# Kernel optimization log

Measured on AMD Instinct MI355X. Metric: run time of the kernel, lower is better.

Reference implementation:

```python
import jax, jax.numpy as jnp
import numpy as np

B, T, C, H, HS = 4, 2048, 384, 6, 64
EPS = 1e-5


def setup_inputs() -> dict:
    key = jax.random.key(0)
    ks = jax.random.split(key, 8)
    s = lambda fan_in: 1.0 / np.sqrt(fan_in)
    return {
        "x": jax.random.normal(ks[0], (B, T, C), jnp.float32),
        "wq": jax.random.normal(ks[1], (H, C, HS), jnp.float32) * s(C),
        "wk": jax.random.normal(ks[2], (H, C, HS), jnp.float32) * s(C),
        "wv": jax.random.normal(ks[3], (H, C, HS), jnp.float32) * s(C),
        "w_proj": jax.random.normal(ks[4], (C, C), jnp.float32) * s(C),
        "b_proj": jnp.zeros((C,), jnp.float32),
        "w1": jax.random.normal(ks[5], (C, 4 * C), jnp.float32) * s(C),
        "b1": jnp.zeros((4 * C,), jnp.float32),
        "w2": jax.random.normal(ks[6], (4 * C, C), jnp.float32) * s(4 * C),
        "b2": jnp.zeros((C,), jnp.float32),
        "g1": jnp.ones((C,), jnp.float32),
        "be1": jnp.zeros((C,), jnp.float32),
        "g2": jnp.ones((C,), jnp.float32),
        "be2": jnp.zeros((C,), jnp.float32),
    }


def _layernorm(z, g, b):
    m = jnp.mean(z, axis=-1, keepdims=True)
    v = jnp.mean((z - m) ** 2, axis=-1, keepdims=True)
    return (z - m) * jax.lax.rsqrt(v + EPS) * g + b


def reference(x, wq, wk, wv, w_proj, b_proj, w1, b1, w2, b2, g1, be1, g2, be2):
    Bx, Tx, Cx = x.shape
    h = _layernorm(x, g1, be1)
    # per-head projections, no bias
    q = jnp.einsum('btc,hcd->bhtd', h, wq)
    k = jnp.einsum('btc,hcd->bhtd', h, wk)
    v = jnp.einsum('btc,hcd->bhtd', h, wv)
    # NOTE: source scales by full embedding dim C, not head_size
    scores = jnp.einsum('bhtd,bhsd->bhts', q, k) * (Cx ** -0.5)
    mask = jnp.tril(jnp.ones((Tx, Tx), bool))  # tril causal mask
    scores = jnp.where(mask[None, None], scores, -jnp.inf)
    # Faithful to source: softmax over dim=1 of (B,T,T) == QUERY axis (axis=2 here)
    w = jax.nn.softmax(scores, axis=2)
    out = jnp.einsum('bhts,bhsd->bhtd', w, v)
    out = out.transpose(0, 2, 1, 3).reshape(Bx, Tx, Cx)  # concat heads
    out = out @ w_proj + b_proj
    x = x + out  # residual 1
    h2 = _layernorm(x, g2, be2)
    f = jax.nn.relu(h2 @ w1 + b1) @ w2 + b2
    return x + f  # residual 2
```

## Files before the change

### kernel.cpp

```cpp
#include <hip/hip_runtime.h>
#include <hip/hip_bf16.h>


#define BB 4
#define TT 2048
#define CC 384
#define HH 6
#define HS 64
#define BT 8192
#define C4 1536
#define VST 2080
#define SCALE 0.05103103630798288f

typedef __attribute__((ext_vector_type(8))) short short8;
typedef __attribute__((ext_vector_type(4))) float f32x4;
typedef __hip_bfloat16 bf16_t;

__device__ inline short8 ld8(const bf16_t* p) { return *reinterpret_cast<const short8*>(p); }
__device__ inline float tof(float v) { return v; }
__device__ inline float tof(bf16_t v) { return __bfloat162float(v); }
__device__ inline short8 cv8(const float* p) {
    f32x4 lo = *(const f32x4*)p;
    f32x4 hi = *(const f32x4*)(p + 4);
    short8 r;
#pragma unroll
    for (int i = 0; i < 4; i++) {
        bf16_t a = __float2bfloat16(lo[i]);
        bf16_t b = __float2bfloat16(hi[i]);
        r[i]     = *reinterpret_cast<short*>(&a);
        r[i + 4] = *reinterpret_cast<short*>(&b);
    }
    return r;
}
#define MFMA(a, b, c) __builtin_amdgcn_mfma_f32_16x16x32_bf16(a, b, c, 0, 0, 0)

__global__ __launch_bounds__(256) void zinit_kernel(float* __restrict__ p, int n4) {
    int i = blockIdx.x * 256 + threadIdx.x;
    if (i < n4) ((f32x4*)p)[i] = (f32x4){0.f, 0.f, 0.f, 0.f};
}

__device__ inline void tc(const float* __restrict__ src, bf16_t* __restrict__ dst,
                          int R, int Cc, int idx) {
    int rc = R * Cc;
    int b = idx / rc;
    int rem = idx - b * rc;
    int c = rem / R;
    int r = rem - c * R;
    dst[b * rc + c * R + r] = __float2bfloat16(src[b * rc + r * Cc + c]);
}
#define RW  147456
#define RW1 589824
#define NTC (3*RW + RW + 2*RW1)
#define NZ  (BT*CC/4)
__global__ __launch_bounds__(256) void prep_kernel(const float* __restrict__ wq,
                                                   const float* __restrict__ wk,
                                                   const float* __restrict__ wv,
                                                   const float* __restrict__ wproj,
                                                   const float* __restrict__ w1,
                                                   const float* __restrict__ w2,
                                                   bf16_t* __restrict__ wall,
                                                   bf16_t* __restrict__ wpt,
                                                   bf16_t* __restrict__ w1t,
                                                   bf16_t* __restrict__ w2t,
                                                   float* __restrict__ attnf) {
    int i = blockIdx.x * 256 + threadIdx.x;
    if (i < RW)                tc(wq, wall, CC, HS, i);
    else if (i < 2*RW)         tc(wk, wall + RW, CC, HS, i - RW);
    else if (i < 3*RW)         tc(wv, wall + 2*RW, CC, HS, i - 2*RW);
    else if (i < 4*RW)         tc(wproj, wpt, CC, CC, i - 3*RW);
    else if (i < 4*RW + RW1)   tc(w1, w1t, CC, C4, i - 4*RW);
    else if (i < NTC)          tc(w2, w2t, C4, CC, i - 4*RW - RW1);
    else {
        int z = i - NTC;
        if (z < NZ) ((f32x4*)attnf)[z] = (f32x4){0.f, 0.f, 0.f, 0.f};
    }
}

template <typename T, bool INIT>
__global__ __launch_bounds__(256) void ln_kernel(const T* __restrict__ x,
                                                 const float* __restrict__ g,
                                                 const float* __restrict__ be,
                                                 bf16_t* __restrict__ out,
                                                 const float* __restrict__ bias2,
                                                 float* __restrict__ oinit) {
    int wave = threadIdx.x >> 6, lane = threadIdx.x & 63;
    int row = blockIdx.x * 4 + wave;
    const T* xr = x + (size_t)row * CC;
    float v[6];
    float s = 0.f;
#pragma unroll
    for (int i = 0; i < 6; i++) { v[i] = tof(xr[lane + i * 64]); s += v[i]; }
#pragma unroll
    for (int off = 32; off > 0; off >>= 1) s += __shfl_xor(s, off, 64);
    float mean = s * (1.f / 384.f);
    float s2 = 0.f;
#pragma unroll
    for (int i = 0; i < 6; i++) { float d = v[i] - mean; s2 += d * d; }
#pragma unroll
    for (int off = 32; off > 0; off >>= 1) s2 += __shfl_xor(s2, off, 64);
    float rstd = rsqrtf(s2 * (1.f / 384.f) + 1e-5f);
    bf16_t* orow = out + (size_t)row * CC;
#pragma unroll
    for (int i = 0; i < 6; i++) {
        int c = lane + i * 64;
        orow[c] = __float2bfloat16((v[i] - mean) * rstd * g[c] + be[c]);
        if constexpr (INIT) oinit[(size_t)row * CC + c] = bias2[c] + v[i];
    }
}

template <int KDIM, int EPI, bool AF32 = false>
__global__ __launch_bounds__(256) void gemm128_kernel(const void* __restrict__ A,
                                                      const bf16_t* __restrict__ Bt,
                                                      const float* __restrict__ bias,
                                                      const void* __restrict__ resid,
                                                      void* __restrict__ o0,
                                                      void* __restrict__ o1,
                                                      void* __restrict__ o2, int N) {
    const int m0 = blockIdx.x * 128, n0 = blockIdx.y * 128;
    const int tid = threadIdx.x;
    const int lane = tid & 63, wave = tid >> 6;
    const int r16 = lane & 15, quad = lane >> 4;
    const int wm = (wave >> 1) * 64, wn = (wave & 1) * 64;
    __shared__ bf16_t Ash[128][40];
    __shared__ bf16_t Bsh[128][40];
    f32x4 zero = {0.f, 0.f, 0.f, 0.f};
    f32x4 acc[4][4];
#pragma unroll
    for (int i = 0; i < 4; i++)
#pragma unroll
        for (int j = 0; j < 4; j++) acc[i][j] = zero;
    const int srow = tid >> 2;
    const int scol = (tid & 3) * 8;
    int kbeg = 0, kend = KDIM;
    if constexpr (EPI == 4) { kbeg = blockIdx.z * (KDIM / 4); kend = kbeg + KDIM / 4; }
    for (int k0 = kbeg; k0 < kend; k0 += 32) {
        short8 a0, a1;
        if constexpr (AF32) {
            const float* Ag = (const float*)A + (size_t)(m0 + srow) * KDIM + k0 + scol;
            a0 = cv8(Ag);
            a1 = cv8(Ag + (size_t)64 * KDIM);
        } else {
            const bf16_t* Ag = (const bf16_t*)A + (size_t)(m0 + srow) * KDIM + k0 + scol;
            a0 = ld8(Ag);
            a1 = ld8(Ag + (size_t)64 * KDIM);
        }
        const bf16_t* Bg = Bt + (size_t)(n0 + srow) * KDIM + k0 + scol;
        short8 b0 = ld8(Bg);
        short8 b1 = ld8(Bg + (size_t)64 * KDIM);
        *(short8*)&Ash[srow][scol]      = a0;
        *(short8*)&Ash[64 + srow][scol] = a1;
        *(short8*)&Bsh[srow][scol]      = b0;
        *(short8*)&Bsh[64 + srow][scol] = b1;
        __syncthreads();
        short8 af[4], bfr[4];
#pragma unroll
        for (int i = 0; i < 4; i++) af[i]  = *(const short8*)&Ash[wm + i * 16 + r16][quad * 8];
#pragma unroll
        for (int i = 0; i < 4; i++) bfr[i] = *(const short8*)&Bsh[wn + i * 16 + r16][quad * 8];
#pragma unroll
        for (int mi = 0; mi < 4; mi++)
#pragma unroll
            for (int ni = 0; ni < 4; ni++)
                acc[mi][ni] = MFMA(af[mi], bfr[ni], acc[mi][ni]);
        __syncthreads();
    }
#pragma unroll
    for (int mi = 0; mi < 4; mi++)
#pragma unroll
        for (int ni = 0; ni < 4; ni++)
#pragma unroll
            for (int reg = 0; reg < 4; reg++) {
                int m = m0 + wm + mi * 16 + quad * 4 + reg;
                int n = n0 + wn + ni * 16 + r16;
                float val = acc[mi][ni][reg];
                if constexpr (EPI == 0) {
                    val += bias[n] + ((const float*)resid)[(size_t)m * N + n];
                    ((bf16_t*)o0)[(size_t)m * N + n] = __float2bfloat16(val);
                } else if constexpr (EPI == 1) {
                    val = fmaxf(val + bias[n], 0.f);
                    ((bf16_t*)o0)[(size_t)m * N + n] = __float2bfloat16(val);
                } else if constexpr (EPI == 2) {
                    val += bias[n] + tof(((const bf16_t*)resid)[(size_t)m * N + n]);
                    ((float*)o0)[(size_t)m * N + n] = val;
                } else if constexpr (EPI == 4) {
                    atomicAdd(&((float*)o0)[(size_t)m * N + n], val);
                } else {
                    int mat = n / 384;
                    int nr  = n - mat * 384;
                    int head = nr >> 6, d = nr & 63;
                    int b = m >> 11, t = m & 2047;
                    int bh = b * HH + head;
                    bf16_t bv = __float2bfloat16(val);
                    if (mat == 0)      ((bf16_t*)o0)[(size_t)(bh * TT + t) * HS + d] = bv;
                    else if (mat == 1) ((bf16_t*)o1)[(size_t)(bh * TT + t) * HS + d] = bv;
                    else               ((bf16_t*)o2)[(size_t)(bh * HS + d) * VST + t] = bv;
                }
            }
}

__global__ __launch_bounds__(256) void colsum_kernel(const bf16_t* __restrict__ qbf,
                                                     const bf16_t* __restrict__ kbf,
                                                     float* __restrict__ colsum) {
    int id = blockIdx.x;
    int bh = (id & 7) + 8 * ((id >> 3) % 3);
    int rem = (id >> 3) / 3;
    int stile = rem & 31, z = rem >> 5;
    if (stile + z * 8 > 31) return;
    int s0 = stile * 64;
    const int lane = threadIdx.x & 63, wave = threadIdx.x >> 6;
    const int r16 = lane & 15, quad = lane >> 4;
    __shared__ bf16_t Ksh[64][72];
    __shared__ float csum[64];
    if (threadIdx.x < 64) csum[threadIdx.x] = 0.f;
    {
        const int srow = threadIdx.x >> 2, scol = (threadIdx.x & 3) << 4;
        const bf16_t* kp = kbf + (size_t)(bh * TT + s0 + srow) * HS + scol;
        *(short8*)&Ksh[srow][scol]     = ld8(kp);
        *(short8*)&Ksh[srow][scol + 8] = ld8(kp + 8);
    }
    __syncthreads();
    short8 bfr[4][2];
#pragma unroll
    for (int ns = 0; ns < 4; ns++)
#pragma unroll
        for (int kk = 0; kk < 2; kk++)
            bfr[ns][kk] = *(const short8*)&Ksh[ns * 16 + r16][kk * 32 + quad * 8];
    float colacc[4] = {0.f, 0.f, 0.f, 0.f};
    for (int jj = wave; jj < 8; jj += 4) {
        int tt = stile + z * 8 + jj;
        if (tt > 31) break;
#pragma unroll
        for (int ms = 0; ms < 4; ms++) {
            const bf16_t* qp = qbf + (size_t)(bh * TT + tt * 64 + ms * 16 + r16) * HS + quad * 8;
            short8 a0 = ld8(qp);
            short8 a1 = ld8(qp + 32);
#pragma unroll
            for (int ns = 0; ns < 4; ns++) {
                f32x4 sacc = {0.f, 0.f, 0.f, 0.f};
                sacc = MFMA(a0, bfr[ns][0], sacc);
                sacc = MFMA(a1, bfr[ns][1], sacc);
#pragma unroll
                for (int reg = 0; reg < 4; reg++) {
                    int t = tt * 64 + ms * 16 + quad * 4 + reg;
                    int s = s0 + ns * 16 + r16;
                    if (s <= t) colacc[ns] += __expf(sacc[reg] * SCALE);
                }
            }
        }
    }
#pragma unroll
    for (int ns = 0; ns < 4; ns++) atomicAdd(&csum[ns * 16 + r16], colacc[ns]);
    __syncthreads();
    if (threadIdx.x < 64) atomicAdd(&colsum[bh * TT + s0 + threadIdx.x], csum[threadIdx.x]);
}

__global__ __launch_bounds__(256) void attn_part_kernel(const bf16_t* __restrict__ qbf,
                                                        const bf16_t* __restrict__ kbf,
                                                        const bf16_t* __restrict__ vst,
                                                        const float* __restrict__ colsum,
                                                        float* __restrict__ attnf) {
    int id = blockIdx.x;
    int bh = (id & 7) + 8 * ((id >> 3) % 3);
    int rem = (id >> 3) / 3;
    int ttile2 = rem & 15, z = rem >> 4;
    int sbeg = z * 8;
    int last = 2 * ttile2 + 1;
    if (sbeg > last) return;
    int send = last + 1 < sbeg + 8 ? last + 1 : sbeg + 8;
    int t0 = ttile2 * 128;
    const int lane = threadIdx.x & 63, wave = threadIdx.x >> 6;
    const int r16 = lane & 15, quad = lane >> 4;
    __shared__ bf16_t Ksh[64][72];
    __shared__ bf16_t Vsh[64][72];
    __shared__ bf16_t El[128][72];
    __shared__ float Crc[64];
    const int srow = threadIdx.x >> 2;
    const int scol = (threadIdx.x & 3) << 4;
    f32x4 zero = {0.f, 0.f, 0.f, 0.f};
    f32x4 oacc[2][4];
#pragma unroll
    for (int mi = 0; mi < 2; mi++)
#pragma unroll
        for (int ns = 0; ns < 4; ns++) oacc[mi][ns] = zero;
    short8 qa[2][2];
#pragma unroll
    for (int mi = 0; mi < 2; mi++) {
        const bf16_t* qp = qbf + (size_t)(bh * TT + t0 + wave * 32 + mi * 16 + r16) * HS + quad * 8;
        qa[mi][0] = ld8(qp);
        qa[mi][1] = ld8(qp + 32);
    }
    for (int st = sbeg; st < send; st++) {
        int s0 = st * 64;
        {
            const bf16_t* kp = kbf + (size_t)(bh * TT + s0 + srow) * HS + scol;
            short8 k0 = ld8(kp);
            short8 k1 = ld8(kp + 8);
            const bf16_t* vp = vst + (size_t)(bh * HS + srow) * VST + s0 + scol;
            short8 v0 = ld8(vp);
            short8 v1 = ld8(vp + 8);
            *(short8*)&Ksh[srow][scol]     = k0;
            *(short8*)&Ksh[srow][scol + 8] = k1;
            *(short8*)&Vsh[srow][scol]     = v0;
            *(short8*)&Vsh[srow][scol + 8] = v1;
            if (threadIdx.x < 64)
                Crc[threadIdx.x] = 1.0f / colsum[bh * TT + s0 + threadIdx.x];
        }
        __syncthreads();
#pragma unroll
        for (int mi = 0; mi < 2; mi++)
#pragma unroll
            for (int ns = 0; ns < 4; ns++) {
                float rc = Crc[ns * 16 + r16];
                f32x4 sacc = zero;
                sacc = MFMA(qa[mi][0], *(const short8*)&Ksh[ns * 16 + r16][quad * 8], sacc);
                sacc = MFMA(qa[mi][1], *(const short8*)&Ksh[ns * 16 + r16][32 + quad * 8], sacc);
#pragma unroll
                for (int reg = 0; reg < 4; reg++) {
                    int t = t0 + wave * 32 + mi * 16 + quad * 4 + reg;
                    int s = s0 + ns * 16 + r16;
                    float e = (s <= t) ? __expf(sacc[reg] * SCALE) * rc : 0.f;
                    El[wave * 32 + mi * 16 + quad * 4 + reg][ns * 16 + r16] = __float2bfloat16(e);
                }
            }
#pragma unroll
        for (int mi = 0; mi < 2; mi++)
#pragma unroll
            for (int ks = 0; ks < 2; ks++) {
                short8 ea = ld8(&El[wave * 32 + mi * 16 + r16][ks * 32 + quad * 8]);
#pragma unroll
                for (int ns = 0; ns < 4; ns++) {
                    short8 vb = *(const short8*)&Vsh[ns * 16 + r16][ks * 32 + quad * 8];
                    oacc[mi][ns] = MFMA(ea, vb, oacc[mi][ns]);
                }
            }
        __syncthreads();
    }
    int b = bh / HH, head = bh - b * HH;
#pragma unroll
    for (int mi = 0; mi < 2; mi++)
#pragma unroll
        for (int ns = 0; ns < 4; ns++)
#pragma unroll
            for (int reg = 0; reg < 4; reg++) {
                int t = t0 + wave * 32 + mi * 16 + quad * 4 + reg;
                int d = ns * 16 + r16;
                atomicAdd(&attnf[(size_t)(b * TT + t) * CC + head * HS + d], oacc[mi][ns][reg]);
            }
}

extern "C" void kernel_launch(void* const* d_in, const int* in_sizes, int n_in,
                              void* d_out, int out_size, void* d_ws, size_t ws_size,
                              hipStream_t stream) {
    const float* x      = (const float*)d_in[0];
    const float* wq     = (const float*)d_in[1];
    const float* wk     = (const float*)d_in[2];
    const float* wv     = (const float*)d_in[3];
    const float* w_proj = (const float*)d_in[4];
    const float* b_proj = (const float*)d_in[5];
    const float* w1     = (const float*)d_in[6];
    const float* b1     = (const float*)d_in[7];
    const float* w2     = (const float*)d_in[8];
    const float* b2     = (const float*)d_in[9];
    const float* g1     = (const float*)d_in[10];
    const float* be1    = (const float*)d_in[11];
    const float* g2     = (const float*)d_in[12];
    const float* be2    = (const float*)d_in[13];
    float* out = (float*)d_out;

    char* p = (char*)d_ws;
    auto alloc = [&](size_t bytes) {
        void* r = (void*)p;
        p += (bytes + 255) & ~(size_t)255;
        return r;
    };
    const size_t ACT  = (size_t)BT * CC * 2;
    bf16_t* wqt    = (bf16_t*)alloc(HH * HS * CC * 2);
    bf16_t* wkt    = (bf16_t*)alloc(HH * HS * CC * 2);
    bf16_t* wvt    = (bf16_t*)alloc(HH * HS * CC * 2);
    bf16_t* wpt    = (bf16_t*)alloc(CC * CC * 2);
    bf16_t* w1t    = (bf16_t*)alloc((size_t)C4 * CC * 2);
    bf16_t* w2t    = (bf16_t*)alloc((size_t)CC * C4 * 2);
    char* slotA = (char*)alloc(ACT);
    char* slotB = (char*)alloc(2 * ACT);
    char* slotC = (char*)alloc((size_t)24 * HS * VST * 2);

    bf16_t* h_bf    = (bf16_t*)slotA;
    bf16_t* h2_bf   = (bf16_t*)slotA;
    bf16_t* q_bf    = (bf16_t*)slotB;
    bf16_t* k_bf    = (bf16_t*)(slotB + ACT);
    bf16_t* f1      = (bf16_t*)slotB;
    bf16_t* v_bf    = (bf16_t*)slotC;
    bf16_t* x1b     = (bf16_t*)slotC;
    float* colsum   = (float*)wqt;
    float* attn_f   = (float*)d_out;
    (void)wkt; (void)wvt;

    prep_kernel<<<(NTC + NZ + 255) / 256, 256, 0, stream>>>(
        wq, wk, wv, w_proj, w1, w2, wqt, wpt, w1t, w2t, attn_f);
    ln_kernel<float, false><<<BT/4, 256, 0, stream>>>(x, g1, be1, h_bf, nullptr, nullptr);
    gemm128_kernel<CC, 3><<<dim3(BT/128, 9), 256, 0, stream>>>(
        h_bf, wqt, nullptr, nullptr, q_bf, k_bf, v_bf, 1152);
    zinit_kernel<<<48, 256, 0, stream>>>(colsum, 24*TT/4);
    colsum_kernel<<<3072, 256, 0, stream>>>(q_bf, k_bf, colsum);
    attn_part_kernel<<<1536, 256, 0, stream>>>(q_bf, k_bf, v_bf, colsum, attn_f);
    gemm128_kernel<CC, 0, true><<<dim3(BT/128, CC/128), 256, 0, stream>>>(
        attn_f, wpt, b_proj, x, x1b, nullptr, nullptr, CC);
    ln_kernel<bf16_t, true><<<BT/4, 256, 0, stream>>>(x1b, g2, be2, h2_bf, b2, out);
    for (int c = 0; c < 2; c++) {
        size_t m0 = (size_t)c * 4096;
        gemm128_kernel<CC, 1><<<dim3(4096/128, C4/128), 256, 0, stream>>>(
            h2_bf + m0 * CC, w1t, b1, nullptr, f1, nullptr, nullptr, C4);
        gemm128_kernel<C4, 4><<<dim3(4096/128, CC/128, 4), 256, 0, stream>>>(
            f1, w2t, nullptr, nullptr, out + m0 * CC, nullptr, nullptr, CC);
    }
}
```

Before: 308.8 us.

## Use LDS-tiled weight transpose in prep and shrink attention score buffer

The per-element weight transpose/convert in the prep kernel is replaced by 64x64 shared-memory tiles with vectorized coalesced loads and stores. The attnf zeroing moves to a separate set of blocks that each store 16 vectors. The attention kernel's El scratch buffer is halved by processing one 16-row query slice at a time, which lowers LDS use and may allow more resident blocks. The tile index math is hard-coded to these shapes.

After: 304.3 us. Within noise of the previous version (-1.5%).

```diff
diff --git a/kernel.cpp b/kernel.cpp
--- a/kernel.cpp
+++ b/kernel.cpp
@@ -39,19 +39,7 @@
     if (i < n4) ((f32x4*)p)[i] = (f32x4){0.f, 0.f, 0.f, 0.f};
 }
 
-__device__ inline void tc(const float* __restrict__ src, bf16_t* __restrict__ dst,
-                          int R, int Cc, int idx) {
-    int rc = R * Cc;
-    int b = idx / rc;
-    int rem = idx - b * rc;
-    int c = rem / R;
-    int r = rem - c * R;
-    dst[b * rc + c * R + r] = __float2bfloat16(src[b * rc + r * Cc + c]);
-}
 #define RW  147456
-#define RW1 589824
-#define NTC (3*RW + RW + 2*RW1)
-#define NZ  (BT*CC/4)
 __global__ __launch_bounds__(256) void prep_kernel(const float* __restrict__ wq,
                                                    const float* __restrict__ wk,
                                                    const float* __restrict__ wv,
@@ -63,16 +51,53 @@
                                                    bf16_t* __restrict__ w1t,
                                                    bf16_t* __restrict__ w2t,
                                                    float* __restrict__ attnf) {
-    int i = blockIdx.x * 256 + threadIdx.x;
-    if (i < RW)                tc(wq, wall, CC, HS, i);
-    else if (i < 2*RW)         tc(wk, wall + RW, CC, HS, i - RW);
-    else if (i < 3*RW)         tc(wv, wall + 2*RW, CC, HS, i - 2*RW);
-    else if (i < 4*RW)         tc(wproj, wpt, CC, CC, i - 3*RW);
-    else if (i < 4*RW + RW1)   tc(w1, w1t, CC, C4, i - 4*RW);
-    else if (i < NTC)          tc(w2, w2t, C4, CC, i - 4*RW - RW1);
-    else {
-        int z = i - NTC;
-        if (z < NZ) ((f32x4*)attnf)[z] = (f32x4){0.f, 0.f, 0.f, 0.f};
+    int id = blockIdx.x;
+    int tid = threadIdx.x;
+    if (id >= 432) {
+        int base = (id - 432) * 256 + tid;
+        f32x4 z = {0.f, 0.f, 0.f, 0.f};
+#pragma unroll
+        for (int k = 0; k < 16; k++)
+            ((f32x4*)attnf)[base + k * 49152] = z;
+        return;
+    }
+    const float* src; bf16_t* dst; int R, C, t;
+    if (id < 108) {
+        int m = id / 36, r = id - m * 36;
+        src = (m == 0 ? wq : (m == 1 ? wk : wv));
+        dst = wall + m * RW;
+        int b = r / 6; t = r - b * 6;
+        src += b * 24576; dst += b * 24576;
+        R = 384; C = 64;
+    } else if (id < 144) { src = wproj; dst = wpt; t = id - 108; R = 384;  C = 384; }
+    else if (id < 288)   { src = w1;    dst = w1t; t = id - 144; R = 384;  C = 1536; }
+    else                 { src = w2;    dst = w2t; t = id - 288; R = 1536; C = 384; }
+    int tiles_r = R >> 6;
+    int tr = t % tiles_r, tc = t / tiles_r;
+    __shared__ float Tsh[64][65];
+    const int rr = tid >> 4;
+    const int cc = (tid & 15) * 4;
+#pragma unroll
+    for (int i = 0; i < 4; i++) {
+        int row = tr * 64 + rr + i * 16;
+        f32x4 v = *(const f32x4*)(src + (size_t)row * C + tc * 64 + cc);
+#pragma unroll
+        for (int j = 0; j < 4; j++) Tsh[rr + i * 16][cc + j] = v[j];
+    }
+    __syncthreads();
+#pragma unroll
+    for (int i = 0; i < 4; i++) {
+        int cl = rr + i * 16;
+        ushort4 o;
+        bf16_t b0 = __float2bfloat16(Tsh[cc + 0][cl]);
+        bf16_t b1 = __float2bfloat16(Tsh[cc + 1][cl]);
+        bf16_t b2v = __float2bfloat16(Tsh[cc + 2][cl]);
+        bf16_t b3 = __float2bfloat16(Tsh[cc + 3][cl]);
+        o.x = *reinterpret_cast<unsigned short*>(&b0);
+        o.y = *reinterpret_cast<unsigned short*>(&b1);
+        o.z = *reinterpret_cast<unsigned short*>(&b2v);
+        o.w = *reinterpret_cast<unsigned short*>(&b3);
+        *(ushort4*)(dst + (size_t)(tc * 64 + cl) * R + tr * 64 + cc) = o;
     }
 }
 
@@ -272,7 +297,7 @@
     const int r16 = lane & 15, quad = lane >> 4;
     __shared__ bf16_t Ksh[64][72];
     __shared__ bf16_t Vsh[64][72];
-    __shared__ bf16_t El[128][72];
+    __shared__ bf16_t El[64][72];
     __shared__ float Crc[64];
     const int srow = threadIdx.x >> 2;
     const int scol = (threadIdx.x & 3) << 4;
@@ -307,7 +332,7 @@
         }
         __syncthreads();
 #pragma unroll
-        for (int mi = 0; mi < 2; mi++)
+        for (int mi = 0; mi < 2; mi++) {
 #pragma unroll
             for (int ns = 0; ns < 4; ns++) {
                 float rc = Crc[ns * 16 + r16];
@@ -319,20 +344,19 @@
                     int t = t0 + wave * 32 + mi * 16 + quad * 4 + reg;
                     int s = s0 + ns * 16 + r16;
                     float e = (s <= t) ? __expf(sacc[reg] * SCALE) * rc : 0.f;
-                    El[wave * 32 + mi * 16 + quad * 4 + reg][ns * 16 + r16] = __float2bfloat16(e);
+                    El[wave * 16 + quad * 4 + reg][ns * 16 + r16] = __float2bfloat16(e);
                 }
             }
 #pragma unroll
-        for (int mi = 0; mi < 2; mi++)
-#pragma unroll
             for (int ks = 0; ks < 2; ks++) {
-                short8 ea = ld8(&El[wave * 32 + mi * 16 + r16][ks * 32 + quad * 8]);
+                short8 ea = ld8(&El[wave * 16 + r16][ks * 32 + quad * 8]);
 #pragma unroll
                 for (int ns = 0; ns < 4; ns++) {
                     short8 vb = *(const short8*)&Vsh[ns * 16 + r16][ks * 32 + quad * 8];
                     oacc[mi][ns] = MFMA(ea, vb, oacc[mi][ns]);
                 }
             }
+        }
         __syncthreads();
     }
     int b = bh / HH, head = bh - b * HH;
@@ -395,7 +419,7 @@
     float* attn_f   = (float*)d_out;
     (void)wkt; (void)wvt;
 
-    prep_kernel<<<(NTC + NZ + 255) / 256, 256, 0, stream>>>(
+    prep_kernel<<<624, 256, 0, stream>>>(
         wq, wk, wv, w_proj, w1, w2, wqt, wpt, w1t, w2t, attn_f);
     ln_kernel<float, false><<<BT/4, 256, 0, stream>>>(x, g1, be1, h_bf, nullptr, nullptr);
     gemm128_kernel<CC, 3><<<dim3(BT/128, 9), 256, 0, stream>>>(
```
